# Kernel optimization log

Hardware: AMD Instinct MI355X
Metric: run time of the kernel (lower is better)

## Reference

```python
import jax, jax.numpy as jnp
import numpy as np

# Mamba2 config (from AdapterMamba: d_model=1024, n_layer=4, headdim=32; mamba_ssm defaults)
D_MODEL = 1024
N_LAYER = 4
EXPAND = 2
HEADDIM = 32
D_STATE = 128
D_CONV = 4
NGROUPS = 1
D_INNER = EXPAND * D_MODEL            # 2048
NHEADS = D_INNER // HEADDIM           # 64
CONV_DIM = D_INNER + 2 * NGROUPS * D_STATE   # 2304
D_IN_PROJ = 2 * D_INNER + 2 * NGROUPS * D_STATE + NHEADS  # 4416
BATCH, SEQLEN = 4, 2048


def setup_inputs() -> dict:
    key = jax.random.key(0)
    ks = jax.random.split(key, 8)
    x = jax.random.normal(ks[0], (BATCH, SEQLEN, D_MODEL), jnp.float32)
    s_in = 1.0 / np.sqrt(D_MODEL)
    s_out = 1.0 / np.sqrt(D_INNER)
    W_in = jax.random.normal(ks[1], (N_LAYER, D_MODEL, D_IN_PROJ), jnp.float32) * s_in
    conv_w = jax.random.normal(ks[2], (N_LAYER, CONV_DIM, D_CONV), jnp.float32) * 0.5
    conv_b = jnp.zeros((N_LAYER, CONV_DIM), jnp.float32)
    # dt_bias = softplus^{-1}(dt) for dt in [1e-3, 0.1] (mamba dt_init)
    dt = jax.random.uniform(ks[3], (N_LAYER, NHEADS), jnp.float32, 0.001, 0.1)
    dt_bias = jnp.log(jnp.expm1(dt))
    # A in [1, 16] per head (A_init_range)
    A_log = jnp.log(jax.random.uniform(ks[4], (N_LAYER, NHEADS), jnp.float32, 1.0, 16.0))
    D = jnp.ones((N_LAYER, NHEADS), jnp.float32)
    gate_norm_w = jnp.ones((N_LAYER, D_INNER), jnp.float32)
    W_out = jax.random.normal(ks[5], (N_LAYER, D_INNER, D_MODEL), jnp.float32) * s_out
    block_norm_w = jnp.ones((N_LAYER, D_MODEL), jnp.float32)
    final_norm_w = jnp.ones((D_MODEL,), jnp.float32)
    return dict(x=x, W_in=W_in, conv_w=conv_w, conv_b=conv_b, dt_bias=dt_bias,
                A_log=A_log, D=D, gate_norm_w=gate_norm_w, W_out=W_out,
                block_norm_w=block_norm_w, final_norm_w=final_norm_w)


def _rmsnorm(x, w, eps=1e-5):
    return x * jax.lax.rsqrt(jnp.mean(x * x, axis=-1, keepdims=True) + eps) * w


def _mamba2_layer(h, Wi, cw, cb, dtb, Alog, Dh, gw, Wo):
    B, L, _ = h.shape
    zxbcdt = h @ Wi                                        # [B,L,4416]
    z, xBC, dt = jnp.split(zxbcdt, [D_INNER, D_INNER + CONV_DIM], axis=-1)
    # causal depthwise conv1d, width D_CONV, over (x, B, C) channels
    xp = jnp.pad(xBC, ((0, 0), (D_CONV - 1, 0), (0, 0)))
    conv = cb + sum(xp[:, k:k + L, :] * cw[:, k] for k in range(D_CONV))
    xBC = jax.nn.silu(conv)
    xs, Bm, Cm = jnp.split(xBC, [D_INNER, D_INNER + D_STATE], axis=-1)
    xs = xs.reshape(B, L, NHEADS, HEADDIM)                 # [B,L,H,P]
    dt = jax.nn.softplus(dt + dtb)                         # [B,L,H]
    A = -jnp.exp(Alog)                                     # [H]
    dA = jnp.exp(dt * A)                                   # [B,L,H]
    dtx = dt[..., None] * xs                               # [B,L,H,P]

    def step(hs, inp):
        dA_t, dtx_t, B_t, C_t = inp
        # hs: [B,H,P,N]
        hs = hs * dA_t[:, :, None, None] + dtx_t[..., None] * B_t[:, None, None, :]
        y = jnp.einsum('bhpn,bn->bhp', hs, C_t)
        return hs, y

    h0 = jnp.zeros((B, NHEADS, HEADDIM, D_STATE), h.dtype)
    _, ys = jax.lax.scan(step, h0, (dA.swapaxes(0, 1), dtx.swapaxes(0, 1),
                                    Bm.swapaxes(0, 1), Cm.swapaxes(0, 1)))
    y = ys.swapaxes(0, 1) + Dh[None, None, :, None] * xs   # skip term D*x
    y = y.reshape(B, L, D_INNER)
    y = _rmsnorm(y * jax.nn.silu(z), gw)                   # gated RMSNorm (Mamba2)
    return y @ Wo


def reference(x, W_in, conv_w, conv_b, dt_bias, A_log, D, gate_norm_w, W_out,
              block_norm_w, final_norm_w):
    h = x
    for l in range(N_LAYER):
        h = h + _mamba2_layer(_rmsnorm(h, block_norm_w[l]), W_in[l], conv_w[l],
                              conv_b[l], dt_bias[l], A_log[l], D[l],
                              gate_norm_w[l], W_out[l])
    return _rmsnorm(h, final_norm_w)
```

## Files before the change

### kernel.cpp

```cpp
#include <hip/hip_runtime.h>

typedef unsigned short u16;
typedef __bf16 bf16x8 __attribute__((ext_vector_type(8)));
typedef float f32x4 __attribute__((ext_vector_type(4)));
typedef u16 u16x8 __attribute__((ext_vector_type(8)));

#define NLAYER 4
#define DMODEL 1024
#define DINNER 2048
#define NHEADS 64
#define CONVDIM 2304
#define XBCLD 2368
#define DPROJ 4416
#define DPROJP 4608
#define BATCH 4
#define SEQLEN 2048
#define NTOK 8192
#define QC 64
#define NCH (SEQLEN / QC)
#define MH 8

__device__ __forceinline__ u16 f2bf(float f) {
  union { float f; unsigned u; } v; v.f = f;
  return (u16)((v.u + 0x7fffu + ((v.u >> 16) & 1u)) >> 16);
}
__device__ __forceinline__ float bf2f(u16 h) {
  union { unsigned u; float f; } v; v.u = (unsigned)h << 16; return v.f;
}

__device__ __forceinline__ float block_sum256(float v) {
  __shared__ float red[4];
  #pragma unroll
  for (int o = 32; o; o >>= 1) v += __shfl_xor(v, o);
  int t = threadIdx.x;
  if ((t & 63) == 0) red[t >> 6] = v;
  __syncthreads();
  return red[0] + red[1] + red[2] + red[3];
}

__device__ __forceinline__ int swz128(int row, int g) { return (row << 7) + (((g ^ (row & 7)) << 3)); }
__device__ __forceinline__ int swz64(int row, int g)  { return (row << 6) + (((g ^ (row & 7)) << 3)); }

#define GLDS16(g, s) __builtin_amdgcn_global_load_lds( \
    (const __attribute__((address_space(1))) void*)(g), \
    (__attribute__((address_space(3))) void*)(s), 16, 0, 0)

template<int MODE>
__global__ __launch_bounds__(256, 2) void gemm2b_k(
    const u16* __restrict__ A, const u16* __restrict__ Bt,
    float* __restrict__ C, u16* __restrict__ zy, u16* __restrict__ xbc,
    float* __restrict__ dtraw, int K, int nkt) {
  __shared__ __align__(16) u16 smem[4 * 8192];

  const int tid = threadIdx.x;
  const int w = tid >> 6, l = tid & 63;
  const int wm = w >> 1, wn = w & 1;
  const int l16 = l & 15, kg = l >> 4;
  const int lr = l >> 3, lc = l & 7;
  const int swg = lc ^ lr;

  const int gx = gridDim.x;
  const int nwg = gx * gridDim.y;
  int bid = blockIdx.y * gx + blockIdx.x;
  bid = (bid & 7) * (nwg >> 3) + (bid >> 3);
  const int m0 = (bid / gx) << 7;
  const int n0 = (bid % gx) << 7;

  f32x4 acc[4][4] = {};

  auto stage = [&](int buf, int kt) {
    const size_t kb = (size_t)(kt << 6) + (swg << 3);
    u16* da = smem + (buf << 13);
    u16* db = smem + ((2 + buf) << 13);
    #pragma unroll
    for (int j = 0; j < 4; ++j) {
      const int r0 = (w << 5) + (j << 3);
      GLDS16(A + (size_t)(m0 + r0 + lr) * K + kb, da + (r0 << 6));
      GLDS16(Bt + (size_t)(n0 + r0 + lr) * K + kb, db + (r0 << 6));
    }
  };
  auto readA = [&](int cur, int mf, int ks) -> bf16x8 {
    const int r = (wm << 6) + (mf << 4) + l16;
    return *(const bf16x8*)&smem[(cur << 13) + (r << 6) + ((((ks << 2) + kg) ^ (r & 7)) << 3)];
  };
  auto readB = [&](int cur, int nf, int ks) -> bf16x8 {
    const int r = (wn << 6) + (nf << 4) + l16;
    return *(const bf16x8*)&smem[((2 + cur) << 13) + (r << 6) + ((((ks << 2) + kg) ^ (r & 7)) << 3)];
  };

  stage(0, 0);
  __syncthreads();

  for (int kt = 0; kt < nkt; ++kt) {
    const int cur = kt & 1;
    if (kt + 1 < nkt) stage(cur ^ 1, kt + 1);
    bf16x8 af[4][2], bq[4][2];
    #pragma unroll
    for (int mf = 0; mf < 4; ++mf)
      #pragma unroll
      for (int ks = 0; ks < 2; ++ks) af[mf][ks] = readA(cur, mf, ks);
    #pragma unroll
    for (int nf = 0; nf < 4; ++nf)
      #pragma unroll
      for (int ks = 0; ks < 2; ++ks) bq[nf][ks] = readB(cur, nf, ks);
    __builtin_amdgcn_s_setprio(1);
    #pragma unroll
    for (int mf = 0; mf < 4; ++mf)
      #pragma unroll
      for (int nf = 0; nf < 4; ++nf)
        #pragma unroll
        for (int ks = 0; ks < 2; ++ks)
          acc[mf][nf] = __builtin_amdgcn_mfma_f32_16x16x32_bf16(
              af[mf][ks], bq[nf][ks], acc[mf][nf], 0, 0, 0);
    __builtin_amdgcn_s_setprio(0);
    __syncthreads();
  }

  if (MODE == 1) {
    const int nt = n0 >> 7;
    if (nt == 35) return;
    if (nt == 34) {
      if (wn == 0) {
        #pragma unroll
        for (int mf = 0; mf < 4; ++mf) {
          const int row = m0 + (wm << 6) + (mf << 4) + (kg << 2);
          #pragma unroll
          for (int nf = 0; nf < 4; ++nf) {
            const int dc = (nf << 4) + l16;
            #pragma unroll
            for (int r = 0; r < 4; ++r)
              dtraw[(size_t)(row + r) * 64 + dc] = acc[mf][nf][r];
          }
        }
      }
      return;
    }
    #pragma unroll
    for (int mf = 0; mf < 4; ++mf)
      #pragma unroll
      for (int nf = 0; nf < 4; ++nf) {
        const int col = (wn << 6) + (nf << 4) + l16;
        #pragma unroll
        for (int r = 0; r < 4; ++r) {
          const int row = (wm << 6) + (mf << 4) + (kg << 2) + r;
          smem[(row << 7) + (((col >> 3) ^ (row & 7)) << 3) + (col & 7)] = f2bf(acc[mf][nf][r]);
        }
      }
    __syncthreads();
    const int g = l & 15;
    #pragma unroll
    for (int j = 0; j < 8; ++j) {
      const int row = (w << 5) + (j << 2) + (l >> 4);
      u16x8 v = *(const u16x8*)&smem[(row << 7) + ((g ^ (row & 7)) << 3)];
      const size_t grow = (size_t)(m0 + row);
      const int gcol = n0 + (g << 3);
      if (nt < 16) *(u16x8*)&zy[grow * DINNER + gcol] = v;
      else         *(u16x8*)&xbc[grow * XBCLD + (gcol - 2048)] = v;
    }
  } else {
    float* smf = (float*)smem;
    #pragma unroll
    for (int mf = 0; mf < 4; ++mf)
      #pragma unroll
      for (int nf = 0; nf < 4; ++nf) {
        const int col = (wn << 6) + (nf << 4) + l16;
        #pragma unroll
        for (int r = 0; r < 4; ++r) {
          const int row = (wm << 6) + (mf << 4) + (kg << 2) + r;
          smf[(row << 7) + ((((col >> 2) ^ (row & 7)) << 2) | (col & 3))] = acc[mf][nf][r];
        }
      }
    __syncthreads();
    const int g = l & 31;
    #pragma unroll
    for (int j = 0; j < 16; ++j) {
      const int row = (w << 5) + (j << 1) + (l >> 5);
      f32x4 v = *(const f32x4*)&smf[(row << 7) + ((g ^ (row & 7)) << 2)];
      float* cp = &C[(size_t)(m0 + row) * DMODEL + n0 + (g << 2)];
      f32x4 o = *(const f32x4*)cp;
      #pragma unroll
      for (int q = 0; q < 4; ++q) o[q] += v[q];
      *(f32x4*)cp = o;
    }
  }
}

__global__ __launch_bounds__(256) void transpose_cvt_k(
    const float* __restrict__ in, u16* __restrict__ out, int R, int Cin, int Cpad) {
  __shared__ float t[64][65];
  const int c0 = blockIdx.x << 6, r0 = blockIdx.y << 6;
  const int tx = threadIdx.x & 63, ty = threadIdx.x >> 6;
  #pragma unroll
  for (int i = 0; i < 16; ++i) {
    int r = ty + (i << 2);
    int cc = c0 + tx;
    t[r][tx] = (cc < Cin) ? in[(size_t)(r0 + r) * Cin + cc] : 0.f;
  }
  __syncthreads();
  #pragma unroll
  for (int i = 0; i < 16; ++i) {
    int c = ty + (i << 2);
    out[(size_t)(c0 + c) * R + r0 + tx] = f2bf(t[tx][c]);
  }
}

__global__ void copy_k(const float* __restrict__ in, float* __restrict__ out, int n4) {
  int i = blockIdx.x * blockDim.x + threadIdx.x;
  int stride = gridDim.x * blockDim.x;
  for (; i < n4; i += stride)
    *(f32x4*)&out[(size_t)i * 4] = *(const f32x4*)&in[(size_t)i * 4];
}

__global__ __launch_bounds__(256) void rmsnorm_bf16_k(
    const float* __restrict__ in, const float* __restrict__ w, u16* __restrict__ out) {
  const size_t row = blockIdx.x;
  const int t = threadIdx.x;
  f32x4 v = *(const f32x4*)&in[row * DMODEL + t * 4];
  float ss = block_sum256(v[0]*v[0] + v[1]*v[1] + v[2]*v[2] + v[3]*v[3]);
  float sc = rsqrtf(ss * (1.f / DMODEL) + 1e-5f);
  f32x4 wv = *(const f32x4*)&w[t * 4];
  ushort4 o;
  o.x = f2bf(v[0] * sc * wv[0]); o.y = f2bf(v[1] * sc * wv[1]);
  o.z = f2bf(v[2] * sc * wv[2]); o.w = f2bf(v[3] * sc * wv[3]);
  *(ushort4*)&out[row * DMODEL + t * 4] = o;
}

__global__ __launch_bounds__(256) void final_rmsnorm_k(
    const float* __restrict__ in, const float* __restrict__ w, float* __restrict__ out) {
  const size_t row = blockIdx.x;
  const int t = threadIdx.x;
  f32x4 v = *(const f32x4*)&in[row * DMODEL + t * 4];
  float ss = block_sum256(v[0]*v[0] + v[1]*v[1] + v[2]*v[2] + v[3]*v[3]);
  float sc = rsqrtf(ss * (1.f / DMODEL) + 1e-5f);
  f32x4 wv = *(const f32x4*)&w[t * 4];
  f32x4 o;
  #pragma unroll
  for (int j = 0; j < 4; ++j) o[j] = v[j] * sc * wv[j];
  *(f32x4*)&out[row * DMODEL + t * 4] = o;
}

__global__ __launch_bounds__(256) void conv_tr_k(
    const u16* __restrict__ xbc, const float* __restrict__ cw,
    const float* __restrict__ cb, u16* __restrict__ xact, u16* __restrict__ BT) {
  __shared__ __align__(16) u16 xin[67][72];
  __shared__ __align__(16) u16 xtr[64][72];
  const int ch0 = blockIdx.x << 6, tok0 = blockIdx.y << 6;
  const int tid = threadIdx.x;
  const bool bstart = (tok0 & (SEQLEN - 1)) == 0;
  {
    const int rr = tid >> 3, sg = (tid & 7) << 3;
    #pragma unroll
    for (int i = 0; i < 2; ++i) {
      int r = rr + (i << 5);
      if (bstart && r < 3) *(u16x8*)&xin[r][sg] = (u16x8){};
      else *(int4*)&xin[r][sg] = *(const int4*)&xbc[(size_t)(tok0 - 3 + r) * XBCLD + ch0 + sg];
    }
    if (tid < 24) {
      int r = 64 + (tid >> 3), s2 = (tid & 7) << 3;
      *(int4*)&xin[r][s2] = *(const int4*)&xbc[(size_t)(tok0 - 3 + r) * XBCLD + ch0 + s2];
    }
  }
  __syncthreads();
  const int c2 = tid & 31, th = tid >> 5;
  const int c = c2 << 1, tb = th << 3;
  float wv[2][4], bias[2];
  #pragma unroll
  for (int cc = 0; cc < 2; ++cc) {
    bias[cc] = cb[ch0 + c + cc];
    #pragma unroll
    for (int k = 0; k < 4; ++k) wv[cc][k] = cw[(ch0 + c + cc) * 4 + k];
  }
  float m3[2], m2[2], m1[2];
  #pragma unroll
  for (int cc = 0; cc < 2; ++cc) {
    m3[cc] = bf2f(xin[tb][c + cc]);
    m2[cc] = bf2f(xin[tb + 1][c + cc]);
    m1[cc] = bf2f(xin[tb + 2][c + cc]);
  }
  u16 ov[8][2];
  #pragma unroll
  for (int j = 0; j < 8; ++j) {
    #pragma unroll
    for (int cc = 0; cc < 2; ++cc) {
      float xc = bf2f(xin[tb + 3 + j][c + cc]);
      float a = bias[cc] + wv[cc][0]*m3[cc] + wv[cc][1]*m2[cc] + wv[cc][2]*m1[cc] + wv[cc][3]*xc;
      ov[j][cc] = f2bf(a / (1.f + expf(-a)));
      m3[cc] = m2[cc]; m2[cc] = m1[cc]; m1[cc] = xc;
    }
    unsigned pk = (unsigned)ov[j][0] | ((unsigned)ov[j][1] << 16);
    *(unsigned*)&xact[(size_t)(tok0 + tb + j) * CONVDIM + ch0 + c] = pk;
  }
  if (ch0 == 2048 || ch0 == 2112) {
    #pragma unroll
    for (int cc = 0; cc < 2; ++cc) {
      u16x8 v;
      #pragma unroll
      for (int j = 0; j < 8; ++j) v[j] = ov[j][cc];
      *(u16x8*)&xtr[c + cc][tb] = v;
    }
    __syncthreads();
    #pragma unroll
    for (int p = 0; p < 2; ++p) {
      int slot = tid + (p << 8);
      int cc2 = slot >> 3, tseg = slot & 7;
      u16x8 v = *(const u16x8*)&xtr[cc2][tseg << 3];
      *(u16x8*)&BT[(size_t)(ch0 - 2048 + cc2) * NTOK + tok0 + (tseg << 3)] = v;
    }
  }
}

__global__ __launch_bounds__(256, 2) void ssd_local_k(
    const u16* __restrict__ xact, const u16* __restrict__ BT,
    const float* __restrict__ dtraw, const float* __restrict__ dt_bias,
    const float* __restrict__ A_log, const float* __restrict__ Dv,
    u16* __restrict__ ybuf, u16* __restrict__ Sg,
    float* __restrict__ etg, float* __restrict__ decayg) {
  __shared__ __align__(16) u16 Bs[64 * 128];
  __shared__ __align__(16) u16 U[128 * 64];
  __shared__ __align__(16) u16 Xa[256 * 64];
  __shared__ __align__(16) u16 Pl[64 * 64];
  __shared__ float cums8[MH][64], dts8[MH][64], fac8[MH][64];

  const int h0 = blockIdx.x << 3, ch = blockIdx.y, b = blockIdx.z;
  const int tid = threadIdx.x, w = tid >> 6, l = tid & 63;
  const int l16 = l & 15, kg = l >> 4;
  const size_t tokb = (size_t)b * SEQLEN + (ch << 6);
  const size_t schunk0 = ((size_t)(b * 64 + h0) << 5) + ch;

  const int srow = tid >> 2, sseg = tid & 3;
  int4 creg[4], breg[4], btreg[4], xreg[MH];
  #pragma unroll
  for (int i = 0; i < 4; ++i) {
    creg[i] = *(const int4*)&xact[(tokb + srow) * CONVDIM + 2176 + (sseg << 5) + (i << 3)];
    breg[i] = *(const int4*)&xact[(tokb + srow) * CONVDIM + 2048 + (sseg << 5) + (i << 3)];
  }
  const int xtt = tid >> 2, xps = tid & 3;
  #pragma unroll
  for (int hh = 0; hh < MH; ++hh)
    xreg[hh] = *(const int4*)&xact[(tokb + xtt) * CONVDIM + ((h0 + hh) << 5) + (xps << 3)];
  #pragma unroll
  for (int i = 0; i < 4; ++i)
    btreg[i] = *(const int4*)&BT[(size_t)(tid >> 1) * NTOK + tokb + ((((tid & 1) << 2) + i) << 3)];

  #pragma unroll
  for (int i = 0; i < 4; ++i) {
    *(int4*)&U[swz128(srow, (sseg << 2) + i)]  = creg[i];
    *(int4*)&Bs[swz128(srow, (sseg << 2) + i)] = breg[i];
  }
  #pragma unroll
  for (int hh = 0; hh < MH; ++hh) {
    u16x8 xv = *(const u16x8*)&xreg[hh];
    #pragma unroll
    for (int j = 0; j < 8; ++j) {
      const int pp = (hh << 5) + (xps << 3) + j;
      Xa[(pp << 6) + ((((xtt >> 3) ^ (pp & 7)) << 3) | (xtt & 7))] = xv[j];
    }
  }

  #pragma unroll
  for (int q = 0; q < 2; ++q) {
    const int hh = (w << 1) + q, hg = h0 + hh;
    const size_t sch = schunk0 + ((size_t)hh << 5);
    float raw = dtraw[(tokb + l) * 64 + hg] + dt_bias[hg];
    float dtv = raw > 20.f ? raw : log1pf(__expf(raw));
    float cv = -dtv * __expf(A_log[hg]);
    #pragma unroll
    for (int d = 1; d < 64; d <<= 1) {
      float o = __shfl_up(cv, d);
      if (l >= d) cv += o;
    }
    float a63 = __shfl(cv, 63);
    cums8[hh][l] = cv; dts8[hh][l] = dtv; fac8[hh][l] = dtv * __expf(a63 - cv);
    etg[(sch << 6) + l] = __expf(cv);
    if (l == 0) decayg[sch] = __expf(a63);
  }
  __syncthreads();

  f32x4 gacc[4] = {};
  #pragma unroll
  for (int ks = 0; ks < 4; ++ks) {
    bf16x8 ac = *(const bf16x8*)&U[swz128((w << 4) + l16, (ks << 2) + kg)];
    #pragma unroll
    for (int j = 0; j < 4; ++j)
      if (j <= w) {
        bf16x8 bb = *(const bf16x8*)&Bs[swz128((j << 4) + l16, (ks << 2) + kg)];
        gacc[j] = __builtin_amdgcn_mfma_f32_16x16x32_bf16(ac, bb, gacc[j], 0, 0, 0);
      }
  }
  __syncthreads();
  #pragma unroll
  for (int i = 0; i < 4; ++i)
    *(int4*)&U[swz64(tid >> 1, ((tid & 1) << 2) + i)] = btreg[i];
  __syncthreads();

  for (int hh = 0; hh < MH; ++hh) {
    const float Dh = Dv[h0 + hh];
    const size_t sch = schunk0 + ((size_t)hh << 5);

    float c_t[4];
    #pragma unroll
    for (int r = 0; r < 4; ++r) c_t[r] = cums8[hh][(w << 4) + (kg << 2) + r];
    #pragma unroll
    for (int j = 0; j < 4; ++j) {
      const int s = (j << 4) + l16;
      const float c_s = cums8[hh][s], d_s = dts8[hh][s];
      #pragma unroll
      for (int r = 0; r < 4; ++r) {
        const int t = (w << 4) + (kg << 2) + r;
        float v = (s <= t) ? gacc[j][r] * __expf(c_t[r] - c_s) * d_s : 0.f;
        Pl[(t << 6) + ((((s >> 3) ^ (t & 7)) << 3) | (s & 7))] = f2bf(v);
      }
    }

    f32x4 y1[2] = {};
    const int nks = (w >> 1) + 1;
    for (int ks = 0; ks < nks; ++ks) {
      bf16x8 ap = *(const bf16x8*)&Pl[swz64((w << 4) + l16, (ks << 2) + kg)];
      #pragma unroll
      for (int pj = 0; pj < 2; ++pj) {
        bf16x8 bx = *(const bf16x8*)&Xa[swz64((hh << 5) + (pj << 4) + l16, (ks << 2) + kg)];
        y1[pj] = __builtin_amdgcn_mfma_f32_16x16x32_bf16(ap, bx, y1[pj], 0, 0, 0);
      }
    }
    #pragma unroll
    for (int r = 0; r < 4; ++r) {
      const int t = (w << 4) + (kg << 2) + r;
      #pragma unroll
      for (int pj = 0; pj < 2; ++pj) {
        const int p = (pj << 4) + l16;
        const int grow = (hh << 5) + p;
        float xv = bf2f(Xa[(grow << 6) + ((((t >> 3) ^ (grow & 7)) << 3) | (t & 7))]);
        ybuf[(tokb + t) * DINNER + ((h0 + hh) << 5) + p] = f2bf(y1[pj][r] + Dh * xv);
      }
    }

    f32x4 sacc[2][2] = {};
    #pragma unroll
    for (int ks = 0; ks < 2; ++ks) {
      float f8[8];
      #pragma unroll
      for (int j = 0; j < 8; ++j) f8[j] = fac8[hh][(ks << 5) + (kg << 3) + j];
      #pragma unroll
      for (int pt = 0; pt < 2; ++pt) {
        bf16x8 xr = *(const bf16x8*)&Xa[swz64((hh << 5) + (pt << 4) + l16, (ks << 2) + kg)];
        bf16x8 xs;
        #pragma unroll
        for (int j = 0; j < 8; ++j) xs[j] = (__bf16)((float)xr[j] * f8[j]);
        #pragma unroll
        for (int nt = 0; nt < 2; ++nt) {
          bf16x8 bb = *(const bf16x8*)&U[swz64(((w << 1) + nt) * 16 + l16, (ks << 2) + kg)];
          sacc[pt][nt] = __builtin_amdgcn_mfma_f32_16x16x32_bf16(xs, bb, sacc[pt][nt], 0, 0, 0);
        }
      }
    }
    u16* sp = Sg + (sch << 12);
    #pragma unroll
    for (int pt = 0; pt < 2; ++pt)
      #pragma unroll
      for (int nt = 0; nt < 2; ++nt)
        #pragma unroll
        for (int r = 0; r < 4; ++r) {
          const int pr = (pt << 4) + (kg << 2) + r;
          const int n = (w << 5) + (nt << 4) + l16;
          sp[(pr << 7) + n] = f2bf(sacc[pt][nt][r]);
        }
  }
}

__global__ __launch_bounds__(256) void state_scan_k(
    u16* __restrict__ SH, const float* __restrict__ decayg) {
  const int bid = blockIdx.x;
  const size_t base = ((size_t)bid << 17) + ((size_t)threadIdx.x << 4);
  float acc[16] = {};
  u16x8 s0 = *(const u16x8*)&SH[base];
  u16x8 s1 = *(const u16x8*)&SH[base + 8];
  for (int ch = 0; ch < 32; ++ch) {
    const float d = decayg[(bid << 5) + ch];
    u16x8 n0 = {}, n1 = {};
    if (ch + 1 < 32) {
      n0 = *(const u16x8*)&SH[base + ((size_t)(ch + 1) << 12)];
      n1 = *(const u16x8*)&SH[base + ((size_t)(ch + 1) << 12) + 8];
    }
    u16x8 h0, h1;
    #pragma unroll
    for (int j = 0; j < 8; ++j) { h0[j] = f2bf(acc[j]); h1[j] = f2bf(acc[8 + j]); }
    *(u16x8*)&SH[base + ((size_t)ch << 12)] = h0;
    *(u16x8*)&SH[base + ((size_t)ch << 12) + 8] = h1;
    #pragma unroll
    for (int j = 0; j < 8; ++j) {
      acc[j]     = d * acc[j]     + bf2f(s0[j]);
      acc[8 + j] = d * acc[8 + j] + bf2f(s1[j]);
    }
    s0 = n0; s1 = n1;
  }
}

__global__ __launch_bounds__(256, 2) void ssd_cross_k(
    const u16* __restrict__ xact, const u16* __restrict__ Hg,
    const float* __restrict__ etg, u16* __restrict__ ybuf) {
  __shared__ __align__(16) u16 Cs[64 * 128];
  __shared__ __align__(16) u16 Hb[32 * 128];
  __shared__ float etl[64];
  const int h0 = blockIdx.x << 3, ch = blockIdx.y + 1, b = blockIdx.z;
  const int tid = threadIdx.x, w = tid >> 6, l = tid & 63;
  const int l16 = l & 15, kg = l >> 4;
  const size_t tokb = (size_t)b * SEQLEN + (ch << 6);
  const size_t schunk0 = ((size_t)(b * 64 + h0) << 5) + ch;

  const int srow = tid >> 2, sseg = tid & 3;
  #pragma unroll
  for (int i = 0; i < 4; ++i) {
    int4 v = *(const int4*)&xact[(tokb + srow) * CONVDIM + 2176 + (sseg << 5) + (i << 3)];
    *(int4*)&Cs[swz128(srow, (sseg << 2) + i)] = v;
  }
  const int hp = tid >> 3, hseg = tid & 7;
  int4 hreg[2];
  float ereg = 0.f;
  #pragma unroll
  for (int i = 0; i < 2; ++i)
    hreg[i] = *(const int4*)&Hg[(schunk0 << 12) + (hp << 7) + (((hseg << 1) + i) << 3)];
  if (tid < 64) ereg = etg[(schunk0 << 6) + tid];
  #pragma unroll
  for (int i = 0; i < 2; ++i) *(int4*)&Hb[swz128(hp, (hseg << 1) + i)] = hreg[i];
  if (tid < 64) etl[tid] = ereg;
  __syncthreads();

  for (int hh = 0; hh < MH; ++hh) {
    if (hh + 1 < MH) {
      const size_t schn = schunk0 + ((size_t)(hh + 1) << 5);
      #pragma unroll
      for (int i = 0; i < 2; ++i)
        hreg[i] = *(const int4*)&Hg[(schn << 12) + (hp << 7) + (((hseg << 1) + i) << 3)];
      if (tid < 64) ereg = etg[(schn << 6) + tid];
    }

    f32x4 y2[2] = {};
    #pragma unroll
    for (int ks = 0; ks < 4; ++ks) {
      bf16x8 ac = *(const bf16x8*)&Cs[swz128((w << 4) + l16, (ks << 2) + kg)];
      #pragma unroll
      for (int pj = 0; pj < 2; ++pj) {
        bf16x8 bh = *(const bf16x8*)&Hb[swz128((pj << 4) + l16, (ks << 2) + kg)];
        y2[pj] = __builtin_amdgcn_mfma_f32_16x16x32_bf16(ac, bh, y2[pj], 0, 0, 0);
      }
    }
    #pragma unroll
    for (int r = 0; r < 4; ++r) {
      const int t = (w << 4) + (kg << 2) + r;
      const float et = etl[t];
      #pragma unroll
      for (int pj = 0; pj < 2; ++pj) {
        const int p = (pj << 4) + l16;
        const size_t a = (tokb + t) * DINNER + ((h0 + hh) << 5) + p;
        ybuf[a] = f2bf(bf2f(ybuf[a]) + et * y2[pj][r]);
      }
    }

    if (hh + 1 < MH) {
      __syncthreads();
      #pragma unroll
      for (int i = 0; i < 2; ++i) *(int4*)&Hb[swz128(hp, (hseg << 1) + i)] = hreg[i];
      if (tid < 64) etl[tid] = ereg;
      __syncthreads();
    }
  }
}

__global__ __launch_bounds__(256) void gate_rmsnorm_k(
    const u16* __restrict__ y, u16* __restrict__ zy, const float* __restrict__ gw) {
  const size_t row = blockIdx.x;
  const int t = threadIdx.x;
  bf16x8 yv = *(const bf16x8*)&y[row * DINNER + t * 8];
  bf16x8 zv = *(const bf16x8*)&zy[row * DINNER + t * 8];
  float val[8]; float ss = 0.f;
  #pragma unroll
  for (int j = 0; j < 8; ++j) {
    float z = (float)zv[j];
    float v = (float)yv[j] * (z / (1.f + expf(-z)));
    val[j] = v; ss += v * v;
  }
  ss = block_sum256(ss);
  float sc = rsqrtf(ss * (1.f / DINNER) + 1e-5f);
  ushort4 o0, o1;
  o0.x = f2bf(val[0]*sc*gw[t*8+0]); o0.y = f2bf(val[1]*sc*gw[t*8+1]);
  o0.z = f2bf(val[2]*sc*gw[t*8+2]); o0.w = f2bf(val[3]*sc*gw[t*8+3]);
  o1.x = f2bf(val[4]*sc*gw[t*8+4]); o1.y = f2bf(val[5]*sc*gw[t*8+5]);
  o1.z = f2bf(val[6]*sc*gw[t*8+6]); o1.w = f2bf(val[7]*sc*gw[t*8+7]);
  *(ushort4*)&zy[row * DINNER + t * 8] = o0;
  *(ushort4*)&zy[row * DINNER + t * 8 + 4] = o1;
}

extern "C" void kernel_launch(void* const* d_in, const int* in_sizes, int n_in,
                              void* d_out, int out_size, void* d_ws, size_t ws_size,
                              hipStream_t stream) {
  const float* x       = (const float*)d_in[0];
  const float* W_in    = (const float*)d_in[1];
  const float* conv_w  = (const float*)d_in[2];
  const float* conv_b  = (const float*)d_in[3];
  const float* dt_bias = (const float*)d_in[4];
  const float* A_log   = (const float*)d_in[5];
  const float* Dv      = (const float*)d_in[6];
  const float* gate_w  = (const float*)d_in[7];
  const float* W_out   = (const float*)d_in[8];
  const float* block_w = (const float*)d_in[9];
  const float* final_w = (const float*)d_in[10];
  float* out = (float*)d_out;

  char* p = (char*)d_ws;
  auto alloc = [&](size_t bytes) { char* r = p; p += (bytes + 255) & ~(size_t)255; return r; };
  float* hbuf  = (float*)alloc((size_t)NTOK * DMODEL * 4);
  u16*   slabA = (u16*)  alloc((size_t)NTOK * DINNER * 2);
  u16*   slabB = (u16*)  alloc((size_t)NTOK * DINNER * 2);
  u16*   slabC = (u16*)  alloc((size_t)NTOK * CONVDIM * 2);
  u16*   xbc   = (u16*)  alloc((size_t)NTOK * XBCLD * 2);
  float* dtraw = (float*)alloc((size_t)NTOK * NHEADS * 4);
  u16*   BT    = (u16*)  alloc((size_t)128 * NTOK * 2);
  if ((size_t)(p - (char*)d_ws) > ws_size) return;

  u16*   Sg     = (u16*)  alloc((size_t)BATCH * NHEADS * NCH * 4096 * 2);
  float* etg    = (float*)alloc((size_t)BATCH * NHEADS * NCH * 64 * 4);
  float* decayg = (float*)alloc((size_t)BATCH * NHEADS * NCH * 4);
  const bool par = ((size_t)(p - (char*)d_ws) <= ws_size);

  u16* hn   = slabA;
  u16* ybuf = slabA;
  u16* wt   = slabC;
  u16* xact = slabC;

  copy_k<<<2048, 256, 0, stream>>>(x, hbuf, NTOK * DMODEL / 4);

  for (int l = 0; l < NLAYER; ++l) {
    rmsnorm_bf16_k<<<NTOK, 256, 0, stream>>>(hbuf, block_w + l * DMODEL, hn);
    transpose_cvt_k<<<dim3(DPROJP/64, DMODEL/64), 256, 0, stream>>>(
        W_in + (size_t)l * DMODEL * DPROJ, wt, DMODEL, DPROJ, DPROJP);
    gemm2b_k<1><<<dim3(DPROJP/128, NTOK/128), 256, 0, stream>>>(
        hn, wt, nullptr, slabB, xbc, dtraw, DMODEL, DMODEL / 64);
    conv_tr_k<<<dim3(CONVDIM/64, NTOK/64), 256, 0, stream>>>(
        xbc, conv_w + (size_t)l * CONVDIM * 4, conv_b + (size_t)l * CONVDIM, xact, BT);
    if (par) {
      ssd_local_k<<<dim3(NHEADS/MH, NCH, BATCH), 256, 0, stream>>>(
          xact, BT, dtraw, dt_bias + l * NHEADS, A_log + l * NHEADS,
          Dv + l * NHEADS, ybuf, Sg, etg, decayg);
      state_scan_k<<<BATCH * NHEADS, 256, 0, stream>>>(Sg, decayg);
      ssd_cross_k<<<dim3(NHEADS/MH, NCH - 1, BATCH), 256, 0, stream>>>(
          xact, Sg, etg, ybuf);
    }
    gate_rmsnorm_k<<<NTOK, 256, 0, stream>>>(ybuf, slabB, gate_w + (size_t)l * DINNER);
    transpose_cvt_k<<<dim3(DMODEL/64, DINNER/64), 256, 0, stream>>>(
        W_out + (size_t)l * DINNER * DMODEL, wt, DINNER, DMODEL, DMODEL);
    gemm2b_k<0><<<dim3(DMODEL/128, NTOK/128), 256, 0, stream>>>(
        slabB, wt, hbuf, nullptr, nullptr, nullptr, DINNER, DINNER / 64);
  }
  final_rmsnorm_k<<<NTOK, 256, 0, stream>>>(hbuf, final_w, out);
}
```

Baseline: 1.334 ms.

## Single-buffer GEMM LDS for higher occupancy and use 64-row tiles for out-proj

The bf16 MFMA GEMM drops LDS double buffering: it keeps one 32KB buffer, synchronises after each stage, and raises launch bounds from 2 to 4 blocks per CU. Latency is meant to be hidden by having more resident workgroups instead of software prefetch. The kernel is now templated on the M-fragment count. The output-projection GEMM uses 64-row tiles, doubling its block count to fill the GPU better. The cost is no intra-block overlap of global loads with MFMA, an extra barrier per k-step, and lower data reuse per tile for the out-proj.

```diff
diff --git a/kernel.cpp b/kernel.cpp
--- a/kernel.cpp
+++ b/kernel.cpp
@@ -45,12 +45,14 @@
     (const __attribute__((address_space(1))) void*)(g), \
     (__attribute__((address_space(3))) void*)(s), 16, 0, 0)
 
-template<int MODE>
-__global__ __launch_bounds__(256, 2) void gemm2b_k(
+template<int MODE, int MF>
+__global__ __launch_bounds__(256, 4) void gemm_sb_k(
     const u16* __restrict__ A, const u16* __restrict__ Bt,
     float* __restrict__ C, u16* __restrict__ zy, u16* __restrict__ xbc,
     float* __restrict__ dtraw, int K, int nkt) {
-  __shared__ __align__(16) u16 smem[4 * 8192];
+  constexpr int BM = MF * 32;
+  constexpr int BOFF = BM * 64;
+  __shared__ __align__(16) u16 smem[16384];
 
   const int tid = threadIdx.x;
   const int w = tid >> 6, l = tid & 63;
@@ -63,49 +65,48 @@
   const int nwg = gx * gridDim.y;
   int bid = blockIdx.y * gx + blockIdx.x;
   bid = (bid & 7) * (nwg >> 3) + (bid >> 3);
-  const int m0 = (bid / gx) << 7;
+  const int m0 = (bid / gx) * BM;
   const int n0 = (bid % gx) << 7;
 
-  f32x4 acc[4][4] = {};
-
-  auto stage = [&](int buf, int kt) {
+  f32x4 acc[MF][4] = {};
+
+  auto stage = [&](int kt) {
     const size_t kb = (size_t)(kt << 6) + (swg << 3);
-    u16* da = smem + (buf << 13);
-    u16* db = smem + ((2 + buf) << 13);
+    #pragma unroll
+    for (int j = 0; j < MF; ++j) {
+      const int r0 = (MF == 4 ? (w << 5) : (w << 4)) + (j << 3);
+      GLDS16(A + (size_t)(m0 + r0 + lr) * K + kb, smem + (r0 << 6));
+    }
     #pragma unroll
     for (int j = 0; j < 4; ++j) {
       const int r0 = (w << 5) + (j << 3);
-      GLDS16(A + (size_t)(m0 + r0 + lr) * K + kb, da + (r0 << 6));
-      GLDS16(Bt + (size_t)(n0 + r0 + lr) * K + kb, db + (r0 << 6));
+      GLDS16(Bt + (size_t)(n0 + r0 + lr) * K + kb, smem + BOFF + (r0 << 6));
     }
   };
-  auto readA = [&](int cur, int mf, int ks) -> bf16x8 {
-    const int r = (wm << 6) + (mf << 4) + l16;
-    return *(const bf16x8*)&smem[(cur << 13) + (r << 6) + ((((ks << 2) + kg) ^ (r & 7)) << 3)];
+  auto readA = [&](int mf, int ks) -> bf16x8 {
+    const int r = wm * (MF << 4) + (mf << 4) + l16;
+    return *(const bf16x8*)&smem[(r << 6) + ((((ks << 2) + kg) ^ (r & 7)) << 3)];
   };
-  auto readB = [&](int cur, int nf, int ks) -> bf16x8 {
+  auto readB = [&](int nf, int ks) -> bf16x8 {
     const int r = (wn << 6) + (nf << 4) + l16;
-    return *(const bf16x8*)&smem[((2 + cur) << 13) + (r << 6) + ((((ks << 2) + kg) ^ (r & 7)) << 3)];
+    return *(const bf16x8*)&smem[BOFF + (r << 6) + ((((ks << 2) + kg) ^ (r & 7)) << 3)];
   };
 
-  stage(0, 0);
-  __syncthreads();
-
   for (int kt = 0; kt < nkt; ++kt) {
-    const int cur = kt & 1;
-    if (kt + 1 < nkt) stage(cur ^ 1, kt + 1);
-    bf16x8 af[4][2], bq[4][2];
-    #pragma unroll
-    for (int mf = 0; mf < 4; ++mf)
-      #pragma unroll
-      for (int ks = 0; ks < 2; ++ks) af[mf][ks] = readA(cur, mf, ks);
+    stage(kt);
+    __syncthreads();
+    bf16x8 af[MF][2], bq[4][2];
+    #pragma unroll
+    for (int mf = 0; mf < MF; ++mf)
+      #pragma unroll
+      for (int ks = 0; ks < 2; ++ks) af[mf][ks] = readA(mf, ks);
     #pragma unroll
     for (int nf = 0; nf < 4; ++nf)
       #pragma unroll
-      for (int ks = 0; ks < 2; ++ks) bq[nf][ks] = readB(cur, nf, ks);
+      for (int ks = 0; ks < 2; ++ks) bq[nf][ks] = readB(nf, ks);
     __builtin_amdgcn_s_setprio(1);
     #pragma unroll
-    for (int mf = 0; mf < 4; ++mf)
+    for (int mf = 0; mf < MF; ++mf)
       #pragma unroll
       for (int nf = 0; nf < 4; ++nf)
         #pragma unroll
@@ -122,8 +123,8 @@
     if (nt == 34) {
       if (wn == 0) {
         #pragma unroll
-        for (int mf = 0; mf < 4; ++mf) {
-          const int row = m0 + (wm << 6) + (mf << 4) + (kg << 2);
+        for (int mf = 0; mf < MF; ++mf) {
+          const int row = m0 + wm * (MF << 4) + (mf << 4) + (kg << 2);
           #pragma unroll
           for (int nf = 0; nf < 4; ++nf) {
             const int dc = (nf << 4) + l16;
@@ -136,13 +137,13 @@
       return;
     }
     #pragma unroll
-    for (int mf = 0; mf < 4; ++mf)
+    for (int mf = 0; mf < MF; ++mf)
       #pragma unroll
       for (int nf = 0; nf < 4; ++nf) {
         const int col = (wn << 6) + (nf << 4) + l16;
         #pragma unroll
         for (int r = 0; r < 4; ++r) {
-          const int row = (wm << 6) + (mf << 4) + (kg << 2) + r;
+          const int row = wm * (MF << 4) + (mf << 4) + (kg << 2) + r;
           smem[(row << 7) + (((col >> 3) ^ (row & 7)) << 3) + (col & 7)] = f2bf(acc[mf][nf][r]);
         }
       }
@@ -160,21 +161,21 @@
   } else {
     float* smf = (float*)smem;
     #pragma unroll
-    for (int mf = 0; mf < 4; ++mf)
+    for (int mf = 0; mf < MF; ++mf)
       #pragma unroll
       for (int nf = 0; nf < 4; ++nf) {
         const int col = (wn << 6) + (nf << 4) + l16;
         #pragma unroll
         for (int r = 0; r < 4; ++r) {
-          const int row = (wm << 6) + (mf << 4) + (kg << 2) + r;
+          const int row = wm * (MF << 4) + (mf << 4) + (kg << 2) + r;
           smf[(row << 7) + ((((col >> 2) ^ (row & 7)) << 2) | (col & 3))] = acc[mf][nf][r];
         }
       }
     __syncthreads();
     const int g = l & 31;
     #pragma unroll
-    for (int j = 0; j < 16; ++j) {
-      const int row = (w << 5) + (j << 1) + (l >> 5);
+    for (int j = 0; j < 8; ++j) {
+      const int row = (w << 4) + (j << 1) + (l >> 5);
       f32x4 v = *(const f32x4*)&smf[(row << 7) + ((g ^ (row & 7)) << 2)];
       float* cp = &C[(size_t)(m0 + row) * DMODEL + n0 + (g << 2)];
       f32x4 o = *(const f32x4*)cp;
@@ -633,7 +634,7 @@
     rmsnorm_bf16_k<<<NTOK, 256, 0, stream>>>(hbuf, block_w + l * DMODEL, hn);
     transpose_cvt_k<<<dim3(DPROJP/64, DMODEL/64), 256, 0, stream>>>(
         W_in + (size_t)l * DMODEL * DPROJ, wt, DMODEL, DPROJ, DPROJP);
-    gemm2b_k<1><<<dim3(DPROJP/128, NTOK/128), 256, 0, stream>>>(
+    gemm_sb_k<1, 4><<<dim3(DPROJP/128, NTOK/128), 256, 0, stream>>>(
         hn, wt, nullptr, slabB, xbc, dtraw, DMODEL, DMODEL / 64);
     conv_tr_k<<<dim3(CONVDIM/64, NTOK/64), 256, 0, stream>>>(
         xbc, conv_w + (size_t)l * CONVDIM * 4, conv_b + (size_t)l * CONVDIM, xact, BT);
@@ -648,7 +649,7 @@
     gate_rmsnorm_k<<<NTOK, 256, 0, stream>>>(ybuf, slabB, gate_w + (size_t)l * DINNER);
     transpose_cvt_k<<<dim3(DMODEL/64, DINNER/64), 256, 0, stream>>>(
         W_out + (size_t)l * DINNER * DMODEL, wt, DINNER, DMODEL, DMODEL);
-    gemm2b_k<0><<<dim3(DMODEL/128, NTOK/128), 256, 0, stream>>>(
+    gemm_sb_k<0, 2><<<dim3(DMODEL/128, NTOK/64), 256, 0, stream>>>(
         slabB, wt, hbuf, nullptr, nullptr, nullptr, DINNER, DINNER / 64);
   }
   final_rmsnorm_k<<<NTOK, 256, 0, stream>>>(hbuf, final_w, out);
```

Result: slower. 2.095 ms (+57.0%).
